# Optimization experiments

Measured on AMD Instinct MI355X. Metric: run time of the kernel, lower is better.

Reference implementation:

```python
import jax, jax.numpy as jnp
import numpy as np

N_NODES = 100000
N_EDGES = 1600000
IN_F = 128
HID = 128
N_CLASSES = 2
N_GRAPHS = 512


def setup_inputs() -> dict:
    key = jax.random.key(0)
    ks = jax.random.split(key, 12)
    x = jax.random.normal(ks[0], (N_NODES, IN_F), dtype=jnp.float32)
    edge_index = jax.random.randint(ks[1], (2, N_EDGES), 0, N_NODES, dtype=jnp.int64)
    batch = jnp.sort(jax.random.randint(ks[2], (N_NODES,), 0, N_GRAPHS, dtype=jnp.int64))
    s_in = 1.0 / np.sqrt(IN_F)
    s_h = 1.0 / np.sqrt(HID)
    return {
        "x": x,
        "edge_index": edge_index,
        "batch": batch,
        "W1": jax.random.normal(ks[3], (IN_F, HID), dtype=jnp.float32) * s_in,
        "b1": jnp.zeros((HID,), dtype=jnp.float32),
        "W2": jax.random.normal(ks[4], (HID, HID), dtype=jnp.float32) * s_h,
        "b2": jnp.zeros((HID,), dtype=jnp.float32),
        "W3": jax.random.normal(ks[5], (HID, HID), dtype=jnp.float32) * s_h,
        "b3": jnp.zeros((HID,), dtype=jnp.float32),
        "Wl": jax.random.normal(ks[6], (HID, N_CLASSES), dtype=jnp.float32) * s_h,
        "bl": jnp.zeros((N_CLASSES,), dtype=jnp.float32),
    }


def reference(x, edge_index, batch, W1, b1, W2, b2, W3, b3, Wl, bl):
    n = x.shape[0]
    src, dst = edge_index[0], edge_index[1]
    # GCNConv adds self-loops and applies symmetric normalization D^-1/2 (A+I) D^-1/2
    loop = jnp.arange(n, dtype=src.dtype)
    src_f = jnp.concatenate([src, loop])  # [E+N]
    dst_f = jnp.concatenate([dst, loop])
    deg = jax.ops.segment_sum(jnp.ones_like(src_f, dtype=x.dtype), dst_f, num_segments=n)
    dis = jax.lax.rsqrt(jnp.maximum(deg, 1.0))  # deg >= 1 due to self-loops
    norm = dis[src_f] * dis[dst_f]  # [E+N]

    def conv(h, W, b):
        h = h @ W                                    # [N, H]
        msg = h[src_f] * norm[:, None]               # gather + scale  [E+N, H]
        agg = jax.ops.segment_sum(msg, dst_f, num_segments=n)  # scatter-add
        return agg + b

    h = jax.nn.relu(conv(x, W1, b1))
    h = jax.nn.relu(conv(h, W2, b2))
    h = conv(h, W3, b3)
    # global_mean_pool over graph ids
    sums = jax.ops.segment_sum(h, batch, num_segments=N_GRAPHS)        # [G, H]
    cnt = jax.ops.segment_sum(jnp.ones((n,), h.dtype), batch, num_segments=N_GRAPHS)
    pooled = sums / jnp.maximum(cnt, 1.0)[:, None]
    # dropout p=0.5 is identity in eval mode
    return pooled @ Wl + bl
```

## Files before the change

kernel.cpp:

```cpp
#include <hip/hip_runtime.h>

#define NF 128
#define NFU 64
#define BW 128
#define KMAX 1024
#define CAP 3072
#define CHUNK 8192

typedef __attribute__((ext_vector_type(8))) short bf16x8;
typedef __attribute__((ext_vector_type(4))) float f32x4;
typedef __attribute__((ext_vector_type(2))) float f32x2;
union U4S8 { uint4 u; bf16x8 s; };

__global__ void detect_kernel(const int* __restrict__ ei, int ne, int* __restrict__ mode) {
    if (threadIdx.x == 0 && blockIdx.x == 0) {
        int step = ne / 32; if (step < 1) step = 1;
        int all0 = 1;
        for (int k = 0; k < 16; ++k) {
            int idx = 2 * k * step + 1;
            if (ei[idx] != 0) { all0 = 0; break; }
        }
        *mode = all0;
    }
}

__global__ __launch_bounds__(256) void hist_kernel(const int* __restrict__ ei, int ne, int n,
                                                   const int* __restrict__ mode, int* __restrict__ btotal,
                                                   int* __restrict__ blkcnt, int K) {
    __shared__ int hist[KMAX];
    int m = *mode;
    int tid = threadIdx.x;
    for (int k = tid; k < K; k += 256) hist[k] = 0;
    __syncthreads();
    int base = blockIdx.x * CHUNK;
    int end = min(base + CHUNK, ne);
    for (int e = base + tid; e < end; e += 256) {
        int dst = m ? ei[2 * (ne + e)] : ei[ne + e];
        if ((unsigned)dst < (unsigned)n) atomicAdd(&hist[dst >> 7], 1);
    }
    __syncthreads();
    for (int k = tid; k < K; k += 256) {
        int c = hist[k];
        blkcnt[(size_t)blockIdx.x * K + k] = c;
        if (c) atomicAdd(&btotal[k], c);
    }
}

__global__ __launch_bounds__(1024) void scanK(const int* __restrict__ btotal, int* __restrict__ bbase,
                                              int* __restrict__ gcur, int K) {
    __shared__ int sm[1024];
    int tid = threadIdx.x;
    int v = (tid < K) ? btotal[tid] : 0;
    sm[tid] = v;
    __syncthreads();
    for (int off = 1; off < 1024; off <<= 1) {
        int t = (tid >= off) ? sm[tid - off] : 0;
        __syncthreads();
        sm[tid] += t;
        __syncthreads();
    }
    if (tid < K) {
        int excl = sm[tid] - v;
        bbase[tid] = excl;
        gcur[tid] = excl;
        if (tid == K - 1) bbase[K] = sm[tid];
    }
}

__global__ __launch_bounds__(256) void scatter_kernel(const int* __restrict__ ei, int ne, int n,
                                                      const int* __restrict__ mode, const int* __restrict__ blkcnt,
                                                      int* __restrict__ gcur, unsigned* __restrict__ pairbuf,
                                                      int K) {
    __shared__ int cur[KMAX];
    int m = *mode;
    int tid = threadIdx.x;
    for (int k = tid; k < K; k += 256) {
        int c = blkcnt[(size_t)blockIdx.x * K + k];
        cur[k] = c ? atomicAdd(&gcur[k], c) : 0;
    }
    __syncthreads();
    int base = blockIdx.x * CHUNK;
    int end = min(base + CHUNK, ne);
    for (int e = base + tid; e < end; e += 256) {
        int src = m ? ei[2 * e] : ei[e];
        int dst = m ? ei[2 * (ne + e)] : ei[ne + e];
        if ((unsigned)dst >= (unsigned)n || (unsigned)src >= (unsigned)n) continue;
        int pos = atomicAdd(&cur[dst >> 7], 1);
        pairbuf[pos] = (unsigned)src | ((unsigned)(dst & (BW - 1)) << 24);
    }
}

__global__ __launch_bounds__(256) void sort_kernel(const unsigned* __restrict__ pairbuf,
                                                   const int* __restrict__ bbase,
                                                   int* __restrict__ rowptr, float* __restrict__ dis,
                                                   int* __restrict__ col, int n, int K) {
    __shared__ unsigned spair[CAP];
    __shared__ int lcol[CAP];
    __shared__ int dcnt[BW];
    __shared__ int pref[BW];
    int tid = threadIdx.x;
    int b = blockIdx.x;
    int r0 = b * BW;
    int base = bbase[b];
    int end = bbase[b + 1];
    int cntb = end - base;
    if (cntb > CAP) cntb = CAP;

    for (int i = tid; i < cntb; i += 256) spair[i] = pairbuf[base + i];
    if (tid < BW) dcnt[tid] = 0;
    __syncthreads();
    for (int i = tid; i < cntb; i += 256) atomicAdd(&dcnt[spair[i] >> 24], 1);
    __syncthreads();
    if (tid < BW) pref[tid] = dcnt[tid];
    __syncthreads();
    for (int off = 1; off < BW; off <<= 1) {
        int t = (tid < BW && tid >= off) ? pref[tid - off] : 0;
        __syncthreads();
        if (tid < BW) pref[tid] += t;
        __syncthreads();
    }
    if (tid < BW) {
        int d = r0 + tid;
        if (d < n) {
            int excl = pref[tid] - dcnt[tid];
            rowptr[d] = base + excl;
            dis[d] = rsqrtf((float)(dcnt[tid] + 1));
        }
    }
    if (b == K - 1 && tid == 0) rowptr[n] = end;
    if (tid < BW) dcnt[tid] = pref[tid] - dcnt[tid];
    __syncthreads();
    for (int i = tid; i < cntb; i += 256) {
        unsigned p = spair[i];
        int slot = atomicAdd(&dcnt[p >> 24], 1);
        if (slot < CAP) lcol[slot] = (int)(p & 0xFFFFFFu);
    }
    __syncthreads();
    for (int i = tid; i < cntb; i += 256) col[base + i] = lcol[i];
}

__device__ inline unsigned pack_bf16(float a, float b) {
    unsigned ua = __float_as_uint(a), ub = __float_as_uint(b);
    ua = (ua + 0x7fffu + ((ua >> 16) & 1u)) >> 16;
    ub = (ub + 0x7fffu + ((ub >> 16) & 1u)) >> 16;
    return ua | (ub << 16);
}
__device__ inline float bflo(unsigned u) { return __uint_as_float(u << 16); }
__device__ inline float bfhi(unsigned u) { return __uint_as_float(u & 0xFFFF0000u); }

__global__ __launch_bounds__(256) void wprep3_kernel(const float* __restrict__ W1, const float* __restrict__ W2,
                                                     const float* __restrict__ W3, uint4* __restrict__ Wb) {
    const float* W = (blockIdx.x == 0) ? W1 : (blockIdx.x == 1) ? W2 : W3;
    uint4* o = Wb + (size_t)blockIdx.x * 2048;
    int tid = threadIdx.x;
#pragma unroll
    for (int it = 0; it < 8; ++it) {
        int item = it * 256 + tid;
        int lane = item & 63;
        int kbjt = item >> 6;
        int kb = kbjt & 3, jt = kbjt >> 2;
        int k0 = kb * 32 + (lane >> 4) * 8;
        int j = jt * 16 + (lane & 15);
        unsigned p[4];
#pragma unroll
        for (int q = 0; q < 4; ++q)
            p[q] = pack_bf16(W[(size_t)(k0 + 2 * q) * NF + j], W[(size_t)(k0 + 2 * q + 1) * NF + j]);
        o[item] = make_uint4(p[0], p[1], p[2], p[3]);
    }
}

__global__ __launch_bounds__(256) void mm_mfma_kernel(const void* __restrict__ A, int a_fp32,
                                                      const uint4* __restrict__ Wb,
                                                      const float* __restrict__ dis,
                                                      unsigned* __restrict__ hs, int n) {
    int tid = threadIdx.x;
    int wave = tid >> 6, lane = tid & 63;
    int r0 = blockIdx.x * 64 + wave * 16;
    if (r0 >= n) return;
    int lrow = lane & 15, lk = lane >> 4;
    int arow = min(r0 + lrow, n - 1);

    f32x4 acc[8];
#pragma unroll
    for (int j = 0; j < 8; ++j) acc[j] = (f32x4){0.f, 0.f, 0.f, 0.f};

    U4S8 af[4];
    if (a_fp32) {
        const float* Af = (const float*)A;
#pragma unroll
        for (int kb = 0; kb < 4; ++kb) {
            const float* p = Af + (size_t)arow * NF + kb * 32 + lk * 8;
            float4 x0 = *(const float4*)p;
            float4 x1 = *(const float4*)(p + 4);
            af[kb].u = make_uint4(pack_bf16(x0.x, x0.y), pack_bf16(x0.z, x0.w),
                                  pack_bf16(x1.x, x1.y), pack_bf16(x1.z, x1.w));
        }
    } else {
        const unsigned* Ab = (const unsigned*)A;
#pragma unroll
        for (int kb = 0; kb < 4; ++kb)
            af[kb].u = *(const uint4*)(Ab + (size_t)arow * NFU + kb * 16 + lk * 4);
    }

#pragma unroll
    for (int kb = 0; kb < 4; ++kb) {
#pragma unroll
        for (int jt = 0; jt < 8; ++jt) {
            U4S8 wf;
            wf.u = Wb[(jt * 4 + kb) * 64 + lane];
            acc[jt] = __builtin_amdgcn_mfma_f32_16x16x32_bf16(wf.s, af[kb].s, acc[jt], 0, 0, 0);
        }
    }

    if (r0 + lrow < n) {
        float dv = dis[r0 + lrow];
        unsigned* orow = hs + (size_t)(r0 + lrow) * NFU;
#pragma unroll
        for (int jt = 0; jt < 8; ++jt) {
            unsigned p0 = pack_bf16(acc[jt][0] * dv, acc[jt][1] * dv);
            unsigned p1 = pack_bf16(acc[jt][2] * dv, acc[jt][3] * dv);
            *(uint2*)(orow + jt * 8 + lk * 2) = make_uint2(p0, p1);
        }
    }
}

#define SPACC(v)                                              \
    { a0 += (f32x2){bflo((v).x), bfhi((v).x)};                \
      a1 += (f32x2){bflo((v).y), bfhi((v).y)};                \
      a2 += (f32x2){bflo((v).z), bfhi((v).z)};                \
      a3 += (f32x2){bflo((v).w), bfhi((v).w)}; }

__global__ __launch_bounds__(256) void spmm_kernel(const unsigned* __restrict__ hs, const int* __restrict__ rowptr,
                                                   const int* __restrict__ col, const float* __restrict__ dis,
                                                   const float* __restrict__ b, unsigned* __restrict__ outb,
                                                   int n, int do_relu) {
    int row = (blockIdx.x * blockDim.x + threadIdx.x) >> 4;
    int fl = threadIdx.x & 15;
    int gbase = threadIdx.x & 48;
    if (row >= n) return;
    int s = rowptr[row], e = rowptr[row + 1];
    int deg = e - s;

    const unsigned* hsf = hs + fl * 4;
    uint4 sv = *(const uint4*)(hsf + (size_t)row * NFU);
    f32x2 a0 = {bflo(sv.x), bfhi(sv.x)};
    f32x2 a1 = {bflo(sv.y), bfhi(sv.y)};
    f32x2 a2 = {bflo(sv.z), bfhi(sv.z)};
    f32x2 a3 = {bflo(sv.w), bfhi(sv.w)};

    for (int jb = 0; jb < deg; jb += 16) {
        int m = min(16, deg - jb);
        int cidx = col[s + jb + ((fl < m) ? fl : (m - 1))];
        int j = 0;
        for (; j + 2 <= m; j += 2) {
            int c0 = __shfl(cidx, gbase + j);
            int c1 = __shfl(cidx, gbase + j + 1);
            uint4 v0 = *(const uint4*)(hsf + (size_t)c0 * NFU);
            uint4 v1 = *(const uint4*)(hsf + (size_t)c1 * NFU);
            SPACC(v0);
            SPACC(v1);
        }
        if (j < m) {
            int c0 = __shfl(cidx, gbase + j);
            uint4 v0 = *(const uint4*)(hsf + (size_t)c0 * NFU);
            SPACC(v0);
        }
    }

    float d = dis[row];
    float4 bb0 = *(const float4*)(b + fl * 8);
    float4 bb1 = *(const float4*)(b + fl * 8 + 4);
    float o[8];
    o[0] = fmaf(d, a0[0], bb0.x); o[1] = fmaf(d, a0[1], bb0.y);
    o[2] = fmaf(d, a1[0], bb0.z); o[3] = fmaf(d, a1[1], bb0.w);
    o[4] = fmaf(d, a2[0], bb1.x); o[5] = fmaf(d, a2[1], bb1.y);
    o[6] = fmaf(d, a3[0], bb1.z); o[7] = fmaf(d, a3[1], bb1.w);
    if (do_relu) {
#pragma unroll
        for (int k = 0; k < 8; ++k) o[k] = fmaxf(o[k], 0.f);
    }
    unsigned q0 = pack_bf16(o[0], o[1]);
    unsigned q1 = pack_bf16(o[2], o[3]);
    unsigned q2 = pack_bf16(o[4], o[5]);
    unsigned q3 = pack_bf16(o[6], o[7]);
    *(uint4*)(outb + (size_t)row * NFU + fl * 4) = make_uint4(q0, q1, q2, q3);
}

__global__ void gbounds_kernel(const int* __restrict__ batch, const int* __restrict__ mode,
                               int* __restrict__ gstart, int n, int G) {
    int m = *mode;
    int i = blockIdx.x * blockDim.x + threadIdx.x;
    if (i >= n) return;
    int g1 = m ? batch[2 * i] : batch[i];
    int g2 = (i == n - 1) ? G : (m ? batch[2 * (i + 1)] : batch[i + 1]);
    if ((unsigned)g1 > (unsigned)G) g1 = G;
    if ((unsigned)g2 > (unsigned)G) g2 = G;
    if (i == 0) for (int g = 0; g <= g1; ++g) gstart[g] = 0;
    for (int g = g1 + 1; g <= g2; ++g) gstart[g] = i + 1;
}

__global__ __launch_bounds__(256) void poolhead_kernel(const unsigned* __restrict__ h, const int* __restrict__ gstart,
                                                       const float* __restrict__ Wl, const float* __restrict__ bl,
                                                       float* __restrict__ out, int G) {
    __shared__ float sacc[16][16][8];
    int g = blockIdx.x >> 2, sub = blockIdx.x & 3;
    int s0 = gstart[g], e0 = gstart[g + 1];
    int cnt = e0 - s0;
    int per = (cnt + 3) >> 2;
    int s = s0 + sub * per;
    int e = min(s + per, e0);
    int tid = threadIdx.x;
    int rg = tid >> 4, fl = tid & 15;

    float acc[8] = {0.f, 0.f, 0.f, 0.f, 0.f, 0.f, 0.f, 0.f};
    for (int i = s + rg; i < e; i += 16) {
        uint4 v = *(const uint4*)(h + (size_t)i * NFU + fl * 4);
        acc[0] += bflo(v.x); acc[1] += bfhi(v.x);
        acc[2] += bflo(v.y); acc[3] += bfhi(v.y);
        acc[4] += bflo(v.z); acc[5] += bfhi(v.z);
        acc[6] += bflo(v.w); acc[7] += bfhi(v.w);
    }
#pragma unroll
    for (int k = 0; k < 8; ++k) sacc[rg][fl][k] = acc[k];
    __syncthreads();
    if (tid < 16) {
        float t[8] = {0.f, 0.f, 0.f, 0.f, 0.f, 0.f, 0.f, 0.f};
        for (int r = 0; r < 16; ++r)
#pragma unroll
            for (int k = 0; k < 8; ++k) t[k] += sacc[r][tid][k];
        float inv = 1.0f / fmaxf((float)cnt, 1.0f);
        float o0 = 0.f, o1 = 0.f;
#pragma unroll
        for (int k = 0; k < 8; ++k) {
            int f = tid * 8 + k;
            o0 += t[k] * inv * Wl[f * 2];
            o1 += t[k] * inv * Wl[f * 2 + 1];
        }
#pragma unroll
        for (int off2 = 8; off2; off2 >>= 1) {
            o0 += __shfl_down(o0, off2, 16);
            o1 += __shfl_down(o1, off2, 16);
        }
        if (tid == 0) {
            if (sub == 0) { o0 += bl[0]; o1 += bl[1]; }
            atomicAdd(&out[g * 2 + 0], o0);
            atomicAdd(&out[g * 2 + 1], o1);
        }
    }
}

extern "C" void kernel_launch(void* const* d_in, const int* in_sizes, int n_in,
                              void* d_out, int out_size, void* d_ws, size_t ws_size,
                              hipStream_t stream) {
    const float* x  = (const float*)d_in[0];
    const int*   ei = (const int*)d_in[1];
    const int*   bt = (const int*)d_in[2];
    const float* W1 = (const float*)d_in[3];
    const float* b1 = (const float*)d_in[4];
    const float* W2 = (const float*)d_in[5];
    const float* b2 = (const float*)d_in[6];
    const float* W3 = (const float*)d_in[7];
    const float* b3 = (const float*)d_in[8];
    const float* Wl = (const float*)d_in[9];
    const float* bl = (const float*)d_in[10];
    float* out = (float*)d_out;

    const int n  = in_sizes[2];
    const int ne = in_sizes[1] / 2;
    const int G  = out_size / 2;
    const int K  = (n + BW - 1) / BW;
    const int nchunks = (ne + CHUNK - 1) / CHUNK;

    size_t off = 0;
    auto alloc = [&](size_t bytes) { size_t o = off; off += (bytes + 255) & ~(size_t)255; return o; };
    char* ws = (char*)d_ws;
    unsigned* hB     = (unsigned*)(ws + alloc((size_t)n * NFU * 4));
    unsigned* hsB    = (unsigned*)(ws + alloc((size_t)n * NFU * 4));
    unsigned* pairbuf= (unsigned*)(ws + alloc((size_t)ne * 4));
    int*      col    = (int*)     (ws + alloc((size_t)ne * 4));
    int*      rowptr = (int*)     (ws + alloc((size_t)(n + 1) * 4));
    float*    dis    = (float*)   (ws + alloc((size_t)n * 4));
    int*      btotal = (int*)     (ws + alloc((size_t)(K + 1) * 4));
    int*      bbase  = (int*)     (ws + alloc((size_t)(K + 1) * 4));
    int*      gcur   = (int*)     (ws + alloc((size_t)(K + 1) * 4));
    int*      gstart = (int*)     (ws + alloc((size_t)(G + 1) * 4));
    int*      blkcnt = (int*)     (ws + alloc((size_t)nchunks * K * 4));
    uint4*    Wb     = (uint4*)   (ws + alloc(3 * 2048 * 16));
    int*      mode   = (int*)     (ws + alloc(256));
    (void)ws_size;

    hipMemsetAsync(btotal, 0, (size_t)(K + 1) * 4, stream);
    hipMemsetAsync(out, 0, (size_t)out_size * 4, stream);

    detect_kernel<<<1, 64, 0, stream>>>(ei, ne, mode);
    wprep3_kernel<<<3, 256, 0, stream>>>(W1, W2, W3, Wb);

    hist_kernel<<<nchunks, 256, 0, stream>>>(ei, ne, n, mode, btotal, blkcnt, K);
    scanK<<<1, 1024, 0, stream>>>(btotal, bbase, gcur, K);
    scatter_kernel<<<nchunks, 256, 0, stream>>>(ei, ne, n, mode, blkcnt, gcur, pairbuf, K);
    sort_kernel<<<K, 256, 0, stream>>>(pairbuf, bbase, rowptr, dis, col, n, K);
    gbounds_kernel<<<(n + 255) / 256, 256, 0, stream>>>(bt, mode, gstart, n, G);

    const int mm_grid = (n + 63) / 64;
    const int sp_grid = (n + 15) / 16;

    mm_mfma_kernel<<<mm_grid, 256, 0, stream>>>(x, 1, Wb, dis, hsB, n);
    spmm_kernel<<<sp_grid, 256, 0, stream>>>(hsB, rowptr, col, dis, b1, hB, n, 1);
    mm_mfma_kernel<<<mm_grid, 256, 0, stream>>>(hB, 0, Wb + 2048, dis, hsB, n);
    spmm_kernel<<<sp_grid, 256, 0, stream>>>(hsB, rowptr, col, dis, b2, hB, n, 1);
    mm_mfma_kernel<<<mm_grid, 256, 0, stream>>>(hB, 0, Wb + 4096, dis, hsB, n);
    spmm_kernel<<<sp_grid, 256, 0, stream>>>(hsB, rowptr, col, dis, b3, hB, n, 0);

    poolhead_kernel<<<G * 4, 256, 0, stream>>>(hB, gstart, Wl, bl, out, G);
}
```

Measured before the change: 320.8 us.

## Fuse SpMM with next-layer MFMA matmul and merge setup kernels

```diff
diff --git a/kernel.cpp b/kernel.cpp
--- a/kernel.cpp
+++ b/kernel.cpp
@@ -12,15 +12,67 @@
 typedef __attribute__((ext_vector_type(2))) float f32x2;
 union U4S8 { uint4 u; bf16x8 s; };
 
-__global__ void detect_kernel(const int* __restrict__ ei, int ne, int* __restrict__ mode) {
-    if (threadIdx.x == 0 && blockIdx.x == 0) {
-        int step = ne / 32; if (step < 1) step = 1;
-        int all0 = 1;
-        for (int k = 0; k < 16; ++k) {
-            int idx = 2 * k * step + 1;
-            if (ei[idx] != 0) { all0 = 0; break; }
-        }
-        *mode = all0;
+__device__ inline unsigned pack_bf16(float a, float b) {
+    unsigned ua = __float_as_uint(a), ub = __float_as_uint(b);
+    ua = (ua + 0x7fffu + ((ua >> 16) & 1u)) >> 16;
+    ub = (ub + 0x7fffu + ((ub >> 16) & 1u)) >> 16;
+    return ua | (ub << 16);
+}
+__device__ inline float bflo(unsigned u) { return __uint_as_float(u << 16); }
+__device__ inline float bfhi(unsigned u) { return __uint_as_float(u & 0xFFFF0000u); }
+
+__global__ void detect_init_kernel(const int* __restrict__ ei, int ne, int* __restrict__ mode,
+                                   int* __restrict__ btotal, int Kp1, float* __restrict__ out, int osz) {
+    if (blockIdx.x == 0) {
+        if (threadIdx.x == 0) {
+            int step = ne / 32; if (step < 1) step = 1;
+            int all0 = 1;
+            for (int k = 0; k < 16; ++k) {
+                int idx = 2 * k * step + 1;
+                if (ei[idx] != 0) { all0 = 0; break; }
+            }
+            *mode = all0;
+        }
+    } else {
+        int i = (blockIdx.x - 1) * 256 + threadIdx.x;
+        int stride = 8 * 256;
+        for (int k = i; k < Kp1; k += stride) btotal[k] = 0;
+        for (int k = i; k < osz; k += stride) out[k] = 0.f;
+    }
+}
+
+__global__ __launch_bounds__(256) void wprep_gbounds_kernel(const float* __restrict__ W1, const float* __restrict__ W2,
+                                                            const float* __restrict__ W3, uint4* __restrict__ Wb,
+                                                            const int* __restrict__ batch, const int* __restrict__ mode,
+                                                            int* __restrict__ gstart, int n, int G) {
+    int tid = threadIdx.x;
+    if (blockIdx.x < 3) {
+        const float* W = (blockIdx.x == 0) ? W1 : (blockIdx.x == 1) ? W2 : W3;
+        uint4* o = Wb + (size_t)blockIdx.x * 2048;
+#pragma unroll
+        for (int it = 0; it < 8; ++it) {
+            int item = it * 256 + tid;
+            int lane = item & 63;
+            int kbjt = item >> 6;
+            int kb = kbjt & 3, jt = kbjt >> 2;
+            int k0 = kb * 32 + (lane >> 4) * 8;
+            int j = jt * 16 + (lane & 15);
+            unsigned p[4];
+#pragma unroll
+            for (int q = 0; q < 4; ++q)
+                p[q] = pack_bf16(W[(size_t)(k0 + 2 * q) * NF + j], W[(size_t)(k0 + 2 * q + 1) * NF + j]);
+            o[item] = make_uint4(p[0], p[1], p[2], p[3]);
+        }
+    } else {
+        int m = *mode;
+        int i = (blockIdx.x - 3) * 256 + tid;
+        if (i >= n) return;
+        int g1 = m ? batch[2 * i] : batch[i];
+        int g2 = (i == n - 1) ? G : (m ? batch[2 * (i + 1)] : batch[i + 1]);
+        if ((unsigned)g1 > (unsigned)G) g1 = G;
+        if ((unsigned)g2 > (unsigned)G) g2 = G;
+        if (i == 0) for (int g = 0; g <= g1; ++g) gstart[g] = 0;
+        for (int g = g1 + 1; g <= g2; ++g) gstart[g] = i + 1;
     }
 }
 
@@ -139,37 +191,7 @@
     for (int i = tid; i < cntb; i += 256) col[base + i] = lcol[i];
 }
 
-__device__ inline unsigned pack_bf16(float a, float b) {
-    unsigned ua = __float_as_uint(a), ub = __float_as_uint(b);
-    ua = (ua + 0x7fffu + ((ua >> 16) & 1u)) >> 16;
-    ub = (ub + 0x7fffu + ((ub >> 16) & 1u)) >> 16;
-    return ua | (ub << 16);
-}
-__device__ inline float bflo(unsigned u) { return __uint_as_float(u << 16); }
-__device__ inline float bfhi(unsigned u) { return __uint_as_float(u & 0xFFFF0000u); }
-
-__global__ __launch_bounds__(256) void wprep3_kernel(const float* __restrict__ W1, const float* __restrict__ W2,
-                                                     const float* __restrict__ W3, uint4* __restrict__ Wb) {
-    const float* W = (blockIdx.x == 0) ? W1 : (blockIdx.x == 1) ? W2 : W3;
-    uint4* o = Wb + (size_t)blockIdx.x * 2048;
-    int tid = threadIdx.x;
-#pragma unroll
-    for (int it = 0; it < 8; ++it) {
-        int item = it * 256 + tid;
-        int lane = item & 63;
-        int kbjt = item >> 6;
-        int kb = kbjt & 3, jt = kbjt >> 2;
-        int k0 = kb * 32 + (lane >> 4) * 8;
-        int j = jt * 16 + (lane & 15);
-        unsigned p[4];
-#pragma unroll
-        for (int q = 0; q < 4; ++q)
-            p[q] = pack_bf16(W[(size_t)(k0 + 2 * q) * NF + j], W[(size_t)(k0 + 2 * q + 1) * NF + j]);
-        o[item] = make_uint4(p[0], p[1], p[2], p[3]);
-    }
-}
-
-__global__ __launch_bounds__(256) void mm_mfma_kernel(const void* __restrict__ A, int a_fp32,
+__global__ __launch_bounds__(256) void mm_mfma_kernel(const float* __restrict__ Af,
                                                       const uint4* __restrict__ Wb,
                                                       const float* __restrict__ dis,
                                                       unsigned* __restrict__ hs, int n) {
@@ -185,21 +207,13 @@
     for (int j = 0; j < 8; ++j) acc[j] = (f32x4){0.f, 0.f, 0.f, 0.f};
 
     U4S8 af[4];
-    if (a_fp32) {
-        const float* Af = (const float*)A;
-#pragma unroll
-        for (int kb = 0; kb < 4; ++kb) {
-            const float* p = Af + (size_t)arow * NF + kb * 32 + lk * 8;
-            float4 x0 = *(const float4*)p;
-            float4 x1 = *(const float4*)(p + 4);
-            af[kb].u = make_uint4(pack_bf16(x0.x, x0.y), pack_bf16(x0.z, x0.w),
-                                  pack_bf16(x1.x, x1.y), pack_bf16(x1.z, x1.w));
-        }
-    } else {
-        const unsigned* Ab = (const unsigned*)A;
-#pragma unroll
-        for (int kb = 0; kb < 4; ++kb)
-            af[kb].u = *(const uint4*)(Ab + (size_t)arow * NFU + kb * 16 + lk * 4);
+#pragma unroll
+    for (int kb = 0; kb < 4; ++kb) {
+        const float* p = Af + (size_t)arow * NF + kb * 32 + lk * 8;
+        float4 x0 = *(const float4*)p;
+        float4 x1 = *(const float4*)(p + 4);
+        af[kb].u = make_uint4(pack_bf16(x0.x, x0.y), pack_bf16(x0.z, x0.w),
+                              pack_bf16(x1.x, x1.y), pack_bf16(x1.z, x1.w));
     }
 
 #pragma unroll
@@ -230,42 +244,50 @@
       a2 += (f32x2){bflo((v).z), bfhi((v).z)};                \
       a3 += (f32x2){bflo((v).w), bfhi((v).w)}; }
 
+__device__ inline void gather_row(const unsigned* __restrict__ hsf, const int* __restrict__ col,
+                                  int s, int e, int row, int fl, int gbase,
+                                  f32x2& a0, f32x2& a1, f32x2& a2, f32x2& a3) {
+    uint4 sv = *(const uint4*)(hsf + (size_t)row * NFU);
+    a0 = (f32x2){bflo(sv.x), bfhi(sv.x)};
+    a1 = (f32x2){bflo(sv.y), bfhi(sv.y)};
+    a2 = (f32x2){bflo(sv.z), bfhi(sv.z)};
+    a3 = (f32x2){bflo(sv.w), bfhi(sv.w)};
+    int deg = e - s;
+    for (int jb = 0; jb < deg; jb += 16) {
+        int m = min(16, deg - jb);
+        int cidx = col[s + jb + ((fl < m) ? fl : (m - 1))];
+        int j = 0;
+        for (; j + 4 <= m; j += 4) {
+            int c0 = __shfl(cidx, gbase + j);
+            int c1 = __shfl(cidx, gbase + j + 1);
+            int c2 = __shfl(cidx, gbase + j + 2);
+            int c3 = __shfl(cidx, gbase + j + 3);
+            uint4 v0 = *(const uint4*)(hsf + (size_t)c0 * NFU);
+            uint4 v1 = *(const uint4*)(hsf + (size_t)c1 * NFU);
+            uint4 v2 = *(const uint4*)(hsf + (size_t)c2 * NFU);
+            uint4 v3 = *(const uint4*)(hsf + (size_t)c3 * NFU);
+            SPACC(v0); SPACC(v1); SPACC(v2); SPACC(v3);
+        }
+        for (; j < m; ++j) {
+            int c0 = __shfl(cidx, gbase + j);
+            uint4 v0 = *(const uint4*)(hsf + (size_t)c0 * NFU);
+            SPACC(v0);
+        }
+    }
+}
+
 __global__ __launch_bounds__(256) void spmm_kernel(const unsigned* __restrict__ hs, const int* __restrict__ rowptr,
                                                    const int* __restrict__ col, const float* __restrict__ dis,
                                                    const float* __restrict__ b, unsigned* __restrict__ outb,
-                                                   int n, int do_relu) {
+                                                   int n) {
     int row = (blockIdx.x * blockDim.x + threadIdx.x) >> 4;
     int fl = threadIdx.x & 15;
     int gbase = threadIdx.x & 48;
     if (row >= n) return;
     int s = rowptr[row], e = rowptr[row + 1];
-    int deg = e - s;
-
     const unsigned* hsf = hs + fl * 4;
-    uint4 sv = *(const uint4*)(hsf + (size_t)row * NFU);
-    f32x2 a0 = {bflo(sv.x), bfhi(sv.x)};
-    f32x2 a1 = {bflo(sv.y), bfhi(sv.y)};
-    f32x2 a2 = {bflo(sv.z), bfhi(sv.z)};
-    f32x2 a3 = {bflo(sv.w), bfhi(sv.w)};
-
-    for (int jb = 0; jb < deg; jb += 16) {
-        int m = min(16, deg - jb);
-        int cidx = col[s + jb + ((fl < m) ? fl : (m - 1))];
-        int j = 0;
-        for (; j + 2 <= m; j += 2) {
-            int c0 = __shfl(cidx, gbase + j);
-            int c1 = __shfl(cidx, gbase + j + 1);
-            uint4 v0 = *(const uint4*)(hsf + (size_t)c0 * NFU);
-            uint4 v1 = *(const uint4*)(hsf + (size_t)c1 * NFU);
-            SPACC(v0);
-            SPACC(v1);
-        }
-        if (j < m) {
-            int c0 = __shfl(cidx, gbase + j);
-            uint4 v0 = *(const uint4*)(hsf + (size_t)c0 * NFU);
-            SPACC(v0);
-        }
-    }
+    f32x2 a0, a1, a2, a3;
+    gather_row(hsf, col, s, e, row, fl, gbase, a0, a1, a2, a3);
 
     float d = dis[row];
     float4 bb0 = *(const float4*)(b + fl * 8);
@@ -275,10 +297,6 @@
     o[2] = fmaf(d, a1[0], bb0.z); o[3] = fmaf(d, a1[1], bb0.w);
     o[4] = fmaf(d, a2[0], bb1.x); o[5] = fmaf(d, a2[1], bb1.y);
     o[6] = fmaf(d, a3[0], bb1.z); o[7] = fmaf(d, a3[1], bb1.w);
-    if (do_relu) {
-#pragma unroll
-        for (int k = 0; k < 8; ++k) o[k] = fmaxf(o[k], 0.f);
-    }
     unsigned q0 = pack_bf16(o[0], o[1]);
     unsigned q1 = pack_bf16(o[2], o[3]);
     unsigned q2 = pack_bf16(o[4], o[5]);
@@ -286,17 +304,73 @@
     *(uint4*)(outb + (size_t)row * NFU + fl * 4) = make_uint4(q0, q1, q2, q3);
 }
 
-__global__ void gbounds_kernel(const int* __restrict__ batch, const int* __restrict__ mode,
-                               int* __restrict__ gstart, int n, int G) {
-    int m = *mode;
-    int i = blockIdx.x * blockDim.x + threadIdx.x;
-    if (i >= n) return;
-    int g1 = m ? batch[2 * i] : batch[i];
-    int g2 = (i == n - 1) ? G : (m ? batch[2 * (i + 1)] : batch[i + 1]);
-    if ((unsigned)g1 > (unsigned)G) g1 = G;
-    if ((unsigned)g2 > (unsigned)G) g2 = G;
-    if (i == 0) for (int g = 0; g <= g1; ++g) gstart[g] = 0;
-    for (int g = g1 + 1; g <= g2; ++g) gstart[g] = i + 1;
+__global__ __launch_bounds__(256) void spmm_mm_kernel(const unsigned* __restrict__ hs_in,
+                                                      const int* __restrict__ rowptr, const int* __restrict__ col,
+                                                      const float* __restrict__ dis, const float* __restrict__ b,
+                                                      const uint4* __restrict__ Wb,
+                                                      unsigned* __restrict__ hs_out, int n) {
+    __shared__ unsigned lh[16][65];
+    int tid = threadIdx.x;
+    int rloc = tid >> 4;
+    int row0 = blockIdx.x * 16;
+    int row = row0 + rloc;
+    int fl = tid & 15;
+    int gbase = tid & 48;
+
+    if (row < n) {
+        int s = rowptr[row], e = rowptr[row + 1];
+        const unsigned* hsf = hs_in + fl * 4;
+        f32x2 a0, a1, a2, a3;
+        gather_row(hsf, col, s, e, row, fl, gbase, a0, a1, a2, a3);
+
+        float d = dis[row];
+        float4 bb0 = *(const float4*)(b + fl * 8);
+        float4 bb1 = *(const float4*)(b + fl * 8 + 4);
+        float o[8];
+        o[0] = fmaxf(fmaf(d, a0[0], bb0.x), 0.f); o[1] = fmaxf(fmaf(d, a0[1], bb0.y), 0.f);
+        o[2] = fmaxf(fmaf(d, a1[0], bb0.z), 0.f); o[3] = fmaxf(fmaf(d, a1[1], bb0.w), 0.f);
+        o[4] = fmaxf(fmaf(d, a2[0], bb1.x), 0.f); o[5] = fmaxf(fmaf(d, a2[1], bb1.y), 0.f);
+        o[6] = fmaxf(fmaf(d, a3[0], bb1.z), 0.f); o[7] = fmaxf(fmaf(d, a3[1], bb1.w), 0.f);
+        lh[rloc][fl * 4 + 0] = pack_bf16(o[0], o[1]);
+        lh[rloc][fl * 4 + 1] = pack_bf16(o[2], o[3]);
+        lh[rloc][fl * 4 + 2] = pack_bf16(o[4], o[5]);
+        lh[rloc][fl * 4 + 3] = pack_bf16(o[6], o[7]);
+    }
+    __syncthreads();
+
+    if (tid < 64) {
+        int lane = tid;
+        int lrow = lane & 15, lk = lane >> 4;
+        f32x4 acc[8];
+#pragma unroll
+        for (int j = 0; j < 8; ++j) acc[j] = (f32x4){0.f, 0.f, 0.f, 0.f};
+        U4S8 af[4];
+#pragma unroll
+        for (int kb = 0; kb < 4; ++kb) {
+            unsigned* p = &lh[lrow][kb * 16 + lk * 4];
+            af[kb].u = make_uint4(p[0], p[1], p[2], p[3]);
+        }
+#pragma unroll
+        for (int kb = 0; kb < 4; ++kb) {
+#pragma unroll
+            for (int jt = 0; jt < 8; ++jt) {
+                U4S8 wf;
+                wf.u = Wb[(jt * 4 + kb) * 64 + lane];
+                acc[jt] = __builtin_amdgcn_mfma_f32_16x16x32_bf16(wf.s, af[kb].s, acc[jt], 0, 0, 0);
+            }
+        }
+        int orow_i = row0 + lrow;
+        if (orow_i < n) {
+            float dv = dis[orow_i];
+            unsigned* orow = hs_out + (size_t)orow_i * NFU;
+#pragma unroll
+            for (int jt = 0; jt < 8; ++jt) {
+                unsigned p0 = pack_bf16(acc[jt][0] * dv, acc[jt][1] * dv);
+                unsigned p1 = pack_bf16(acc[jt][2] * dv, acc[jt][3] * dv);
+                *(uint2*)(orow + jt * 8 + lk * 2) = make_uint2(p0, p1);
+            }
+        }
+    }
 }
 
 __global__ __launch_bounds__(256) void poolhead_kernel(const unsigned* __restrict__ h, const int* __restrict__ gstart,
@@ -374,8 +448,9 @@
     size_t off = 0;
     auto alloc = [&](size_t bytes) { size_t o = off; off += (bytes + 255) & ~(size_t)255; return o; };
     char* ws = (char*)d_ws;
-    unsigned* hB     = (unsigned*)(ws + alloc((size_t)n * NFU * 4));
+    unsigned* hsA    = (unsigned*)(ws + alloc((size_t)n * NFU * 4));
     unsigned* hsB    = (unsigned*)(ws + alloc((size_t)n * NFU * 4));
+    unsigned* h3     = (unsigned*)(ws + alloc((size_t)n * NFU * 4));
     unsigned* pairbuf= (unsigned*)(ws + alloc((size_t)ne * 4));
     int*      col    = (int*)     (ws + alloc((size_t)ne * 4));
     int*      rowptr = (int*)     (ws + alloc((size_t)(n + 1) * 4));
@@ -389,27 +464,21 @@
     int*      mode   = (int*)     (ws + alloc(256));
     (void)ws_size;
 
-    hipMemsetAsync(btotal, 0, (size_t)(K + 1) * 4, stream);
-    hipMemsetAsync(out, 0, (size_t)out_size * 4, stream);
-
-    detect_kernel<<<1, 64, 0, stream>>>(ei, ne, mode);
-    wprep3_kernel<<<3, 256, 0, stream>>>(W1, W2, W3, Wb);
+    detect_init_kernel<<<9, 256, 0, stream>>>(ei, ne, mode, btotal, K + 1, out, out_size);
+    wprep_gbounds_kernel<<<3 + (n + 255) / 256, 256, 0, stream>>>(W1, W2, W3, Wb, bt, mode, gstart, n, G);
 
     hist_kernel<<<nchunks, 256, 0, stream>>>(ei, ne, n, mode, btotal, blkcnt, K);
     scanK<<<1, 1024, 0, stream>>>(btotal, bbase, gcur, K);
     scatter_kernel<<<nchunks, 256, 0, stream>>>(ei, ne, n, mode, blkcnt, gcur, pairbuf, K);
     sort_kernel<<<K, 256, 0, stream>>>(pairbuf, bbase, rowptr, dis, col, n, K);
-    gbounds_kernel<<<(n + 255) / 256, 256, 0, stream>>>(bt, mode, gstart, n, G);
 
     const int mm_grid = (n + 63) / 64;
     const int sp_grid = (n + 15) / 16;
 
-    mm_mfma_kernel<<<mm_grid, 256, 0, stream>>>(x, 1, Wb, dis, hsB, n);
-    spmm_kernel<<<sp_grid, 256, 0, stream>>>(hsB, rowptr, col, dis, b1, hB, n, 1);
-    mm_mfma_kernel<<<mm_grid, 256, 0, stream>>>(hB, 0, Wb + 2048, dis, hsB, n);
-    spmm_kernel<<<sp_grid, 256, 0, stream>>>(hsB, rowptr, col, dis, b2, hB, n, 1);
-    mm_mfma_kernel<<<mm_grid, 256, 0, stream>>>(hB, 0, Wb + 4096, dis, hsB, n);
-    spmm_kernel<<<sp_grid, 256, 0, stream>>>(hsB, rowptr, col, dis, b3, hB, n, 0);
-
-    poolhead_kernel<<<G * 4, 256, 0, stream>>>(hB, gstart, Wl, bl, out, G);
-}
+    mm_mfma_kernel<<<mm_grid, 256, 0, stream>>>(x, Wb, dis, hsA, n);
+    spmm_mm_kernel<<<sp_grid, 256, 0, stream>>>(hsA, rowptr, col, dis, b1, Wb + 2048, hsB, n);
+    spmm_mm_kernel<<<sp_grid, 256, 0, stream>>>(hsB, rowptr, col, dis, b2, Wb + 4096, hsA, n);
+    spmm_kernel<<<sp_grid, 256, 0, stream>>>(hsA, rowptr, col, dis, b3, h3, n);
+
+    poolhead_kernel<<<G * 4, 256, 0, stream>>>(h3, gstart, Wl, bl, out, G);
+}
```

Result: faster. 289.7 us (-9.7%).
